# Kernel tuning notes

Hardware: AMD Instinct MI355X
Metric: run time of the kernel (lower is better)

Reference implementation:

```python
import jax, jax.numpy as jnp
import numpy as np
from jax import lax

TEMPERATURE = 0.0005


def conv1d(x, w, b, pad):
    # x: [B, Cin, T], w: [Cout, Cin, K], b: [Cout]
    y = lax.conv_general_dilated(x, w, window_strides=(1,), padding=[(pad, pad)],
                                 dimension_numbers=('NCH', 'OIH', 'NCH'))
    return y + b[None, :, None]


def setup_inputs() -> dict:
    key = jax.random.key(0)
    ks = jax.random.split(key, 16)
    B, Cq, Ck, Ca, Tde, Ten = 32, 80, 512, 80, 2000, 400

    def xavier(k, shape):
        fan_in = shape[1] * (shape[2] if len(shape) > 2 else 1)
        fan_out = shape[0] * (shape[2] if len(shape) > 2 else 1)
        lim = float(np.sqrt(6.0 / (fan_in + fan_out)))
        return jax.random.uniform(k, shape, jnp.float32, -lim, lim)

    inp = {
        'queries': jax.random.normal(ks[0], (B, Cq, Tde), jnp.float32),
        'keys': jax.random.normal(ks[1], (B, Ck, Ten), jnp.float32),
        'mask': jnp.ones((B, 1, Ten), jnp.int32),
        # key_layer: Conv(512->1024,k3,p1) -> ReLU -> Conv(1024->80,k1)
        'kw1': xavier(ks[2], (Ck * 2, Ck, 3)), 'kb1': jnp.zeros((Ck * 2,), jnp.float32),
        'kw2': xavier(ks[3], (Ca, Ck * 2, 1)), 'kb2': jnp.zeros((Ca,), jnp.float32),
        # query_layer: Conv(80->160,k3,p1)->ReLU->Conv(160->80,k1)->ReLU->Conv(80->80,k1)
        'qw1': xavier(ks[4], (Cq * 2, Cq, 3)), 'qb1': jnp.zeros((Cq * 2,), jnp.float32),
        'qw2': xavier(ks[5], (Cq, Cq * 2, 1)), 'qb2': jnp.zeros((Cq,), jnp.float32),
        'qw3': xavier(ks[6], (Ca, Cq, 1)), 'qb3': jnp.zeros((Ca,), jnp.float32),
    }
    return inp


def reference(queries, keys, mask, kw1, kb1, kw2, kb2, qw1, qb1, qw2, qb2, qw3, qb3):
    # key path: conv3 -> relu -> conv1
    k = conv1d(jax.nn.relu(conv1d(keys, kw1, kb1, 1)), kw2, kb2, 0)          # [B,Ca,Ten]
    # query path: conv3 -> relu -> conv1 -> relu -> conv1
    q = conv1d(queries, qw1, qb1, 1)
    q = jax.nn.relu(conv1d(jax.nn.relu(q), qw2, qb2, 0))
    q = conv1d(q, qw3, qb3, 0)                                               # [B,Ca,Tde]

    # sum_c (q - k)^2 = |q|^2 + |k|^2 - 2 q.k  (avoids [B,C,Tde,Ten] intermediate)
    q2 = jnp.sum(q * q, axis=1)                      # [B,Tde]
    k2 = jnp.sum(k * k, axis=1)                      # [B,Ten]
    qk = jnp.einsum('bcd,bce->bde', q, k)            # [B,Tde,Ten]
    dist = q2[:, :, None] + k2[:, None, :] - 2.0 * qk
    attn_logp = (-TEMPERATURE * dist)[:, None]       # [B,1,Tde,Ten]

    # masked fill over encoder positions (softmax dim)
    m = mask.astype(bool)[:, :, None, :]             # [B,1,1,Ten]
    attn_logp = jnp.where(m, attn_logp, -jnp.inf)
    attn = jax.nn.softmax(attn_logp, axis=3)
    return attn, attn_logp
```

## Files before the change

kernel.cpp:

```cpp
#include <hip/hip_runtime.h>
#include <hip/hip_bf16.h>
#include <math.h>

#define NB 32
#define CK 512
#define C1 1024
#define CA 80
#define CQ 80
#define CQ2 160
#define TEN 400
#define TDE 2000
#define KDIM 1536
#define TPAD 448
#define TQP 2048

static constexpr float TEMP = 0.0005f;

typedef __attribute__((ext_vector_type(8))) short short8;
typedef __attribute__((ext_vector_type(4))) float f32x4;

__device__ inline short f2bf(float v) {
  __hip_bfloat16 h = __float2bfloat16(v);
  return *(short*)&h;
}
__device__ inline float bf2f(short s) {
  __hip_bfloat16 h = *(__hip_bfloat16*)&s;
  return __bfloat162float(h);
}

__device__ inline void gload_lds16(const void* g, void* l) {
  __builtin_amdgcn_global_load_lds(
      (const __attribute__((address_space(1))) unsigned int*)g,
      (__attribute__((address_space(3))) unsigned int*)l, 16, 0, 0);
}


__device__ void cvt_weights_body(
    int i0, const float* __restrict__ kw1, const float* __restrict__ kw2,
    const float* __restrict__ qw1, const float* __restrict__ qw2,
    const float* __restrict__ qw3, short* __restrict__ w1bf,
    short* __restrict__ w2bf, short* __restrict__ w1q,
    short* __restrict__ w2q, short* __restrict__ w3q) {
  int i = i0 * 256 + threadIdx.x;
  if (i < 1572864) {
    w1bf[i] = f2bf(kw1[i]);
    return;
  }
  i -= 1572864;
  if (i < 131072) {
    int r = i >> 10, c = i & 1023;
    w2bf[i] = f2bf(r < CA ? kw2[r * 1024 + c] : 0.f);
    return;
  }
  i -= 131072;
  if (i < 49152) {
    int r = i >> 8, c = i & 255;
    w1q[i] = f2bf((r < CQ2 && c < 240) ? qw1[r * 240 + c] : 0.f);
    return;
  }
  i -= 49152;
  if (i < 20480) {
    int r = i / 160, c = i - r * 160;
    w2q[i] = f2bf(r < CA ? qw2[r * 160 + c] : 0.f);
    return;
  }
  i -= 20480;
  if (i < 12288) {
    int r = i / 96, c = i - r * 96;
    w3q[i] = f2bf((r < CA && c < CQ) ? qw3[r * 80 + c] : 0.f);
  }
}

__device__ void im2col_k_body(int idx, const float* __restrict__ keys,
                              short* __restrict__ BmatT, float* sq ) {
  const int t0 = (idx % 7) * 64;
  const int b = idx / 7;
  const int tid = threadIdx.x;
  for (int ci0 = 0; ci0 < CK; ci0 += 64) {
    for (int k = tid; k < 64 * 66; k += 256) {
      int c = k / 66, j = k % 66;
      int t = t0 - 1 + j;
      sq[c * 66 + j] =
          (t >= 0 && t < TEN) ? keys[((size_t)b * CK + ci0 + c) * TEN + t] : 0.f;
    }
    __syncthreads();
    for (int k = tid; k < 64 * 24; k += 256) {
      int j = k / 24, seg = k % 24;
      if (t0 + j < TEN) {
        short8 v;
        #pragma unroll
        for (int u = 0; u < 8; ++u) {
          int kk = seg * 8 + u;
          int ci = kk / 3, dk = kk - ci * 3;
          v[u] = f2bf(sq[ci * 66 + j + dk]);
        }
        *(short8*)(BmatT + ((size_t)b * TPAD + t0 + j) * KDIM + ci0 * 3 + seg * 8) = v;
      }
    }
    __syncthreads();
  }
}

__device__ void im2col_q_body(int idx, const float* __restrict__ queries,
                              short* __restrict__ Bq, float* sq ) {
  const int t0 = (idx & 31) * 64;
  const int b = idx >> 5;
  const int tid = threadIdx.x;
  for (int k = tid; k < 80 * 66; k += 256) {
    int c = k / 66, j = k % 66;
    int t = t0 - 1 + j;
    sq[c * 66 + j] =
        (t >= 0 && t < TDE) ? queries[((size_t)b * CQ + c) * TDE + t] : 0.f;
  }
  __syncthreads();
  for (int k = tid; k < 64 * 32; k += 256) {
    int j = k >> 5, seg = k & 31;
    const bool live = (t0 + j) < TDE;
    short8 v;
    #pragma unroll
    for (int u = 0; u < 8; ++u) {
      int kk = seg * 8 + u;
      float f = 0.f;
      if (live && kk < 240) {
        int ci = kk / 3, dk = kk - ci * 3;
        f = sq[ci * 66 + j + dk];
      }
      v[u] = f2bf(f);
    }
    *(short8*)(Bq + ((size_t)b * TQP + t0 + j) * 256 + seg * 8) = v;
  }
}

template <int MODE, bool RELU>
__device__ void qgemm_body(int bx, int by, int bz,
                           const short* __restrict__ A, const short* __restrict__ B,
                           const float* __restrict__ bias, void* __restrict__ outv,
                           int M, int Kpad, int kiters, int Nvalid, int outCols,
                           size_t bBatchStride, size_t outBatchStride, int outLD,
                           short* A_lds , short* B_lds ) {
  const int co0 = bx * 64;
  const int t0  = by * 64;
  const int b   = bz;
  const int tid = threadIdx.x;
  const int l = tid & 63, w = tid >> 6;
  const int srow = tid >> 2, sslot = tid & 3;

  const short* gA = A + (size_t)(co0 + srow) * Kpad + sslot * 8;
  const short* gB = B + (size_t)b * bBatchStride + (size_t)(t0 + srow) * Kpad + sslot * 8;
  const int wbyte = (srow * 64 + sslot * 16) ^ ((srow & 7) << 4);

  const int kslot = l >> 4;
  const int arow = w * 16 + (l & 15);
  const int abyte = (arow * 64 + kslot * 16) ^ ((arow & 7) << 4);
  int bbyte[4];
  #pragma unroll
  for (int g = 0; g < 4; ++g) {
    int brow = g * 16 + (l & 15);
    bbyte[g] = (brow * 64 + kslot * 16) ^ ((brow & 7) << 4);
  }

  f32x4 acc[4];
  #pragma unroll
  for (int g = 0; g < 4; ++g) acc[g] = (f32x4){0.f, 0.f, 0.f, 0.f};

  uint4 av = *(const uint4*)gA;
  uint4 bv = *(const uint4*)gB;
  for (int kt = 0; kt < kiters; ++kt) {
    __syncthreads();
    *(uint4*)((char*)A_lds + wbyte) = av;
    *(uint4*)((char*)B_lds + wbyte) = bv;
    __syncthreads();
    uint4 an = av, bn = bv;
    if (kt + 1 < kiters) {
      an = *(const uint4*)(gA + (kt + 1) * 32);
      bn = *(const uint4*)(gB + (kt + 1) * 32);
    }
    short8 a = *(const short8*)((const char*)A_lds + abyte);
    #pragma unroll
    for (int g = 0; g < 4; ++g) {
      short8 bb = *(const short8*)((const char*)B_lds + bbyte[g]);
      acc[g] = __builtin_amdgcn_mfma_f32_16x16x32_bf16(a, bb, acc[g], 0, 0, 0);
    }
    av = an; bv = bn;
  }

  #pragma unroll
  for (int g = 0; g < 4; ++g) {
    int t = t0 + g * 16 + (l & 15);
    if (t >= Nvalid) continue;
    #pragma unroll
    for (int r = 0; r < 4; ++r) {
      int co = co0 + w * 16 + kslot * 4 + r;
      if (MODE == 1) {
        if (co < outCols) {
          float v = 0.f;
          if (co < M) {
            v = acc[g][r] + bias[co];
            if (RELU) v = v > 0.f ? v : 0.f;
          }
          ((short*)outv)[(size_t)b * outBatchStride + (size_t)t * outLD + co] = f2bf(v);
        }
      } else {
        if (co < M) {
          float v = acc[g][r] + bias[co];
          if (RELU) v = v > 0.f ? v : 0.f;
          ((float*)outv)[(size_t)b * outBatchStride + (size_t)co * outLD + t] = v;
        }
      }
    }
  }
}


__global__ __launch_bounds__(256) void stageA_kernel(
    const float* __restrict__ kw1, const float* __restrict__ kw2,
    const float* __restrict__ qw1, const float* __restrict__ qw2,
    const float* __restrict__ qw3, short* __restrict__ w1bf,
    short* __restrict__ w2bf, short* __restrict__ w1q,
    short* __restrict__ w2q, short* __restrict__ w3q,
    const float* __restrict__ keys, short* __restrict__ BmatT) {
  __shared__ float sq[64 * 66];
  int flat = blockIdx.x;
  if (flat < 6976) {
    cvt_weights_body(flat, kw1, kw2, qw1, qw2, qw3, w1bf, w2bf, w1q, w2q, w3q);
  } else {
    im2col_k_body(flat - 6976, keys, BmatT, sq);
  }
}

__global__ __launch_bounds__(256) void kconv1_mfma_kernel(
    const short* __restrict__ w1bf, const short* __restrict__ BmatT,
    const float* __restrict__ b1, short* __restrict__ k1t) {
  __shared__ short A_lds[8192];
  __shared__ short B_lds[8192];
  const int flat = blockIdx.x;
  const int cox = flat >> 7;
  const int rem = flat & 127;
  const int b   = rem >> 2;
  const int ty  = rem & 3;
  const int co0 = cox * 128;
  const int t0  = ty * 128;
  const int tid = threadIdx.x;
  const int l = tid & 63, w = tid >> 6;

  const short* gsrc[8];
  short* ldst[8];
  #pragma unroll
  for (int j = 0; j < 8; ++j) {
    int c = w * 8 + j;
    int Y = (c & 15) * 1024 + l * 16;
    int X = Y ^ (((Y >> 7) & 7) << 4);
    int row = X >> 7, slot = (X >> 4) & 7;
    if (c < 16) {
      gsrc[j] = w1bf + (size_t)(co0 + row) * KDIM + slot * 8;
      ldst[j] = &A_lds[(c & 15) * 512];
    } else {
      int gr = t0 + row;
      if (gr > TPAD - 1) gr = TPAD - 1;
      gsrc[j] = BmatT + ((size_t)b * TPAD + gr) * KDIM + slot * 8;
      ldst[j] = &B_lds[(c & 15) * 512];
    }
  }

  const int kslot = l >> 4;
  const int li15 = l & 15;
  int abyte[2][2], bbyte[8][2];
  #pragma unroll
  for (int i = 0; i < 2; ++i) {
    int arow = w * 32 + i * 16 + li15;
    #pragma unroll
    for (int kk = 0; kk < 2; ++kk)
      abyte[i][kk] = (arow * 128 + kk * 64 + kslot * 16) ^ ((arow & 7) << 4);
  }
  #pragma unroll
  for (int g = 0; g < 8; ++g) {
    int brow = g * 16 + li15;
    #pragma unroll
    for (int kk = 0; kk < 2; ++kk)
      bbyte[g][kk] = (brow * 128 + kk * 64 + kslot * 16) ^ ((brow & 7) << 4);
  }

  f32x4 acc[2][8];
  #pragma unroll
  for (int i = 0; i < 2; ++i)
    #pragma unroll
    for (int g = 0; g < 8; ++g) acc[i][g] = (f32x4){0.f, 0.f, 0.f, 0.f};

  for (int kt = 0; kt < KDIM / 64; ++kt) {
    __syncthreads();
    #pragma unroll
    for (int j = 0; j < 8; ++j) gload_lds16(gsrc[j] + kt * 64, ldst[j]);
    __syncthreads();
    #pragma unroll
    for (int kk = 0; kk < 2; ++kk) {
      short8 a0 = *(const short8*)((const char*)A_lds + abyte[0][kk]);
      short8 a1 = *(const short8*)((const char*)A_lds + abyte[1][kk]);
      #pragma unroll
      for (int g = 0; g < 8; ++g) {
        short8 bb = *(const short8*)((const char*)B_lds + bbyte[g][kk]);
        acc[0][g] = __builtin_amdgcn_mfma_f32_16x16x32_bf16(a0, bb, acc[0][g], 0, 0, 0);
        acc[1][g] = __builtin_amdgcn_mfma_f32_16x16x32_bf16(a1, bb, acc[1][g], 0, 0, 0);
      }
    }
  }

  #pragma unroll
  for (int g = 0; g < 8; ++g) {
    int t = t0 + g * 16 + li15;
    if (t < TEN) {
      #pragma unroll
      for (int i = 0; i < 2; ++i) {
        #pragma unroll
        for (int r = 0; r < 4; ++r) {
          int co = co0 + w * 32 + i * 16 + kslot * 4 + r;
          float v = acc[i][g][r] + b1[co];
          k1t[((size_t)b * TPAD + t) * C1 + co] = f2bf(v > 0.f ? v : 0.f);
        }
      }
    }
  }
}

__global__ __launch_bounds__(256) void stageC_kernel(
    const float* __restrict__ queries, short* __restrict__ Bq,
    const short* __restrict__ w2bf, const short* __restrict__ k1t,
    const float* __restrict__ kb2, short* __restrict__ kB) {
  __shared__ __align__(16) char pool[21120];
  int flat = blockIdx.x;
  if (flat < 1024) {
    im2col_q_body(flat, queries, Bq, (float*)pool);
  } else {
    int j = flat - 1024;
    int bx = j & 1, rest = j >> 1;
    int by = rest % 7, bz = rest / 7;
    qgemm_body<1, false>(bx, by, bz, w2bf, k1t, kb2, kB, CA, C1, 32, TEN, 96,
                         (size_t)TPAD * C1, (size_t)TPAD * 96, 96,
                         (short*)pool, (short*)(pool + 4096));
  }
}

template <int MODE, bool RELU>
__global__ __launch_bounds__(256) void qgemm_kernel(
    const short* __restrict__ A, const short* __restrict__ B,
    const float* __restrict__ bias, void* __restrict__ outv,
    int M, int Kpad, int kiters, int Nvalid, int outCols,
    size_t bBatchStride, size_t outBatchStride, int outLD) {
  __shared__ short A_lds[2048];
  __shared__ short B_lds[2048];
  qgemm_body<MODE, RELU>(blockIdx.x, blockIdx.y, blockIdx.z, A, B, bias, outv,
                         M, Kpad, kiters, Nvalid, outCols, bBatchStride,
                         outBatchStride, outLD, A_lds, B_lds);
}

__global__ __launch_bounds__(256) void attn_fused_kernel(
    const short* __restrict__ qA, const short* __restrict__ kB,
    const int* __restrict__ mask, float* __restrict__ out_attn,
    float* __restrict__ out_logp) {
  __shared__ short A_lds[3][2048];
  __shared__ short B_lds[3][2560];
  __shared__ float k2LDS[400];
  __shared__ float q2row[64];
  __shared__ int mLDS[400];
  const int t0 = blockIdx.x * 64;
  const int b  = blockIdx.y;
  const int tid = threadIdx.x;
  const int l = tid & 63, w = tid >> 6;

  {
    const int arow_s = tid >> 2, aslot = tid & 3;
    const short* gA = qA + ((size_t)b * TQP + t0 + arow_s) * 96 + aslot * 8;
    #pragma unroll
    for (int p = 0; p < 3; ++p) {
      uint4 v = *(const uint4*)(gA + p * 32);
      *(uint4*)((char*)&A_lds[p][0] +
                ((arow_s * 64 + aslot * 16) ^ ((arow_s & 7) << 4))) = v;
    }
  }
  for (int idx = tid; idx < 400; idx += 256) {
    mLDS[idx] = mask[(size_t)b * TEN + idx];
  }

  const int kslot = l >> 4;
  const int arow = w * 16 + (l & 15);
  const int abyte = (arow * 64 + kslot * 16) ^ ((arow & 7) << 4);

  f32x4 acc[25];
  #pragma unroll
  for (int i = 0; i < 25; ++i) acc[i] = (f32x4){0.f, 0.f, 0.f, 0.f};

  __syncthreads();

  {
    int row = tid >> 2, g = tid & 3;
    float s = 0.f;
    #pragma unroll
    for (int q3i = 0; q3i < 3; ++q3i) {
      int q = 3 * g + q3i;
      int p = q >> 2, slot = q & 3;
      int byteo = (row * 64 + slot * 16) ^ ((row & 7) << 4);
      short8 v = *(const short8*)((const char*)&A_lds[p][0] + byteo);
      #pragma unroll
      for (int u = 0; u < 8; ++u) { float f = bf2f(v[u]); s += f * f; }
    }
    s += __shfl_xor(s, 1, 64);
    s += __shfl_xor(s, 2, 64);
    if (g == 0) q2row[row] = s;
  }

  #pragma unroll
  for (int st = 0; st < 5; ++st) {
    for (int idx = tid; idx < 960; idx += 256) {
      int row = idx / 12, c = idx - row * 12;
      int panel = c >> 2, ps = c & 3;
      uint4 v = *(const uint4*)(kB + ((size_t)b * TPAD + st * 80 + row) * 96 + c * 8);
      *(uint4*)((char*)&B_lds[panel][0] +
                ((row * 64 + ps * 16) ^ ((row & 7) << 4))) = v;
    }
    __syncthreads();
    if (tid < 160) {
      int row = tid >> 1, h = tid & 1;
      float s = 0.f;
      #pragma unroll
      for (int qi = 0; qi < 6; ++qi) {
        int q = 6 * h + qi;
        int p = q >> 2, slot = q & 3;
        int byteo = (row * 64 + slot * 16) ^ ((row & 7) << 4);
        short8 v = *(const short8*)((const char*)&B_lds[p][0] + byteo);
        #pragma unroll
        for (int u = 0; u < 8; ++u) { float f = bf2f(v[u]); s += f * f; }
      }
      s += __shfl_xor(s, 1, 64);
      if (h == 0) k2LDS[st * 80 + row] = s;
    }
    #pragma unroll
    for (int kt = 0; kt < 3; ++kt) {
      short8 a = *(const short8*)((const char*)&A_lds[kt][0] + abyte);
      #pragma unroll
      for (int f = 0; f < 5; ++f) {
        int brow = f * 16 + (l & 15);
        short8 bb = *(const short8*)((const char*)&B_lds[kt][0] +
                                     ((brow * 64 + kslot * 16) ^ ((brow & 7) << 4)));
        acc[st * 5 + f] =
            __builtin_amdgcn_mfma_f32_16x16x32_bf16(a, bb, acc[st * 5 + f], 0, 0, 0);
      }
    }
    __syncthreads();
  }

  int trow[4]; float q2v[4];
  #pragma unroll
  for (int r = 0; r < 4; ++r) {
    trow[r] = t0 + w * 16 + kslot * 4 + r;
    q2v[r] = q2row[w * 16 + kslot * 4 + r];
  }
  #pragma unroll
  for (int sf = 0; sf < 25; ++sf) {
    int s = sf * 16 + (l & 15);
    float k2v = k2LDS[s];
    bool mk = mLDS[s] != 0;
    #pragma unroll
    for (int r = 0; r < 4; ++r) {
      float lp = mk ? (-TEMP) * (q2v[r] + k2v - 2.f * acc[sf][r]) : -INFINITY;
      acc[sf][r] = lp;
    }
  }
  #pragma unroll
  for (int r = 0; r < 4; ++r) {
    if (trow[r] < TDE) {
      float* dst = out_logp + ((size_t)(b * TDE + trow[r])) * TEN + (l & 15);
      #pragma unroll
      for (int sf = 0; sf < 25; ++sf) dst[sf * 16] = acc[sf][r];
    }
  }
  float m[4];
  #pragma unroll
  for (int r = 0; r < 4; ++r) m[r] = -INFINITY;
  #pragma unroll
  for (int sf = 0; sf < 25; ++sf)
    #pragma unroll
    for (int r = 0; r < 4; ++r) m[r] = fmaxf(m[r], acc[sf][r]);
  #pragma unroll
  for (int o = 1; o < 16; o <<= 1)
    #pragma unroll
    for (int r = 0; r < 4; ++r) m[r] = fmaxf(m[r], __shfl_xor(m[r], o, 64));
  float sum[4] = {0.f, 0.f, 0.f, 0.f};
  #pragma unroll
  for (int sf = 0; sf < 25; ++sf)
    #pragma unroll
    for (int r = 0; r < 4; ++r) {
      float v = acc[sf][r];
      float e = (v != -INFINITY) ? __expf(v - m[r]) : 0.f;
      acc[sf][r] = e;
      sum[r] += e;
    }
  #pragma unroll
  for (int o = 1; o < 16; o <<= 1)
    #pragma unroll
    for (int r = 0; r < 4; ++r) sum[r] += __shfl_xor(sum[r], o, 64);
  float inv[4];
  #pragma unroll
  for (int r = 0; r < 4; ++r) inv[r] = 1.0f / sum[r];
  #pragma unroll
  for (int r = 0; r < 4; ++r) {
    if (trow[r] < TDE) {
      float* dst = out_attn + ((size_t)(b * TDE + trow[r])) * TEN + (l & 15);
      #pragma unroll
      for (int sf = 0; sf < 25; ++sf) dst[sf * 16] = acc[sf][r] * inv[r];
    }
  }
}

extern "C" void kernel_launch(void* const* d_in, const int* in_sizes, int n_in,
                              void* d_out, int out_size, void* d_ws, size_t ws_size,
                              hipStream_t stream) {
  const float* queries = (const float*)d_in[0];
  const float* keys    = (const float*)d_in[1];
  const int*   mask    = (const int*)d_in[2];
  const float* kw1 = (const float*)d_in[3];
  const float* kb1 = (const float*)d_in[4];
  const float* kw2 = (const float*)d_in[5];
  const float* kb2 = (const float*)d_in[6];
  const float* qw1 = (const float*)d_in[7];
  const float* qb1 = (const float*)d_in[8];
  const float* qw2 = (const float*)d_in[9];
  const float* qb2 = (const float*)d_in[10];
  const float* qw3 = (const float*)d_in[11];
  const float* qb3 = (const float*)d_in[12];
  float* out = (float*)d_out;

  char* ws = (char*)d_ws;
  short* BmatT = (short*)ws;
  short* w1bf  = (short*)(ws + 44040192);
  short* k1t   = (short*)(ws + 47185920);
  short* w2bf  = (short*)(ws + 76546048);
  short* w1q   = (short*)(ws + 76808192);
  short* w2q   = (short*)(ws + 76906496);
  short* w3q   = (short*)(ws + 76947456);
  short* Bq    = (short*)ws;
  short* q1bf  = (short*)(ws + 33554432);
  short* q2bf  = (short*)(ws + 54525952);
  short* qA    = (short*)(ws + 20480000);
  short* kB    = (short*)(ws + 81920000);

  const long long HALF = 25600000LL;
  float* out_attn = out;
  float* out_logp = out + HALF;

  stageA_kernel<<<dim3(7200), dim3(256), 0, stream>>>(
      kw1, kw2, qw1, qw2, qw3, w1bf, w2bf, w1q, w2q, w3q, keys, BmatT);

  kconv1_mfma_kernel<<<dim3(1024), dim3(256), 0, stream>>>(w1bf, BmatT, kb1, k1t);

  stageC_kernel<<<dim3(1472), dim3(256), 0, stream>>>(
      queries, Bq, w2bf, k1t, kb2, kB);

  qgemm_kernel<1, true><<<dim3(3, TQP / 64, NB), dim3(256), 0, stream>>>(
      w1q, Bq, qb1, q1bf, CQ2, 256, 8, TQP, 160,
      (size_t)TQP * 256, (size_t)TQP * 160, 160);
  qgemm_kernel<1, true><<<dim3(2, TQP / 64, NB), dim3(256), 0, stream>>>(
      w2q, q1bf, qb2, q2bf, CA, 160, 5, TQP, 96,
      (size_t)TQP * 160, (size_t)TQP * 96, 96);
  qgemm_kernel<1, false><<<dim3(2, TQP / 64, NB), dim3(256), 0, stream>>>(
      w3q, q2bf, qb3, qA, CA, 96, 3, TQP, 96,
      (size_t)TQP * 96, (size_t)TQP * 96, 96);

  attn_fused_kernel<<<dim3(TQP / 64, NB), dim3(256), 0, stream>>>(
      qA, kB, mask, out_attn, out_logp);
}
```

Measured before the change: 329.6 us.

## Double-buffer LDS tiles in key conv1 GEMM with halved K step

The key-path conv1 MFMA kernel now keeps two LDS buffers for the A and B tiles. Global-to-LDS loads for the next K slice are issued while MFMAs run on the current one, so each iteration needs one barrier instead of two. The K step drops from 64 to 32 to keep LDS use the same. The XOR swizzle and its inverse are rewritten for the narrower 64-byte rows. In exchange there are twice as many loop iterations, each with less work to hide the barrier and load latency behind.

```diff
diff --git a/kernel.cpp b/kernel.cpp
--- a/kernel.cpp
+++ b/kernel.cpp
@@ -231,8 +231,8 @@
 __global__ __launch_bounds__(256) void kconv1_mfma_kernel(
     const short* __restrict__ w1bf, const short* __restrict__ BmatT,
     const float* __restrict__ b1, short* __restrict__ k1t) {
-  __shared__ short A_lds[8192];
-  __shared__ short B_lds[8192];
+  __shared__ short A_lds[2][4096];
+  __shared__ short B_lds[2][4096];
   const int flat = blockIdx.x;
   const int cox = flat >> 7;
   const int rem = flat & 127;
@@ -243,41 +243,47 @@
   const int tid = threadIdx.x;
   const int l = tid & 63, w = tid >> 6;
 
-  const short* gsrc[8];
-  short* ldst[8];
-  #pragma unroll
-  for (int j = 0; j < 8; ++j) {
-    int c = w * 8 + j;
-    int Y = (c & 15) * 1024 + l * 16;
-    int X = Y ^ (((Y >> 7) & 7) << 4);
-    int row = X >> 7, slot = (X >> 4) & 7;
-    if (c < 16) {
+  auto invswz = [](int Y) {
+    int X = Y;
+    X ^= ((Y >> 8) & 1) << 6;
+    X ^= ((Y >> 7) & 1) << 5;
+    X ^= (((Y >> 6) ^ (Y >> 8)) & 1) << 4;
+    return X;
+  };
+
+  const short* gsrc[4];
+  int ldoff[4];
+  bool isA[4];
+  #pragma unroll
+  for (int j = 0; j < 4; ++j) {
+    int c = w * 4 + j;
+    int Y = (c & 7) * 1024 + l * 16;
+    int X = invswz(Y);
+    int row = X >> 6, slot = (X >> 4) & 3;
+    isA[j] = (c < 8);
+    ldoff[j] = (c & 7) * 512;
+    if (c < 8) {
       gsrc[j] = w1bf + (size_t)(co0 + row) * KDIM + slot * 8;
-      ldst[j] = &A_lds[(c & 15) * 512];
     } else {
       int gr = t0 + row;
       if (gr > TPAD - 1) gr = TPAD - 1;
       gsrc[j] = BmatT + ((size_t)b * TPAD + gr) * KDIM + slot * 8;
-      ldst[j] = &B_lds[(c & 15) * 512];
     }
   }
 
   const int kslot = l >> 4;
   const int li15 = l & 15;
-  int abyte[2][2], bbyte[8][2];
+  int abyte[2];
   #pragma unroll
   for (int i = 0; i < 2; ++i) {
     int arow = w * 32 + i * 16 + li15;
-    #pragma unroll
-    for (int kk = 0; kk < 2; ++kk)
-      abyte[i][kk] = (arow * 128 + kk * 64 + kslot * 16) ^ ((arow & 7) << 4);
-  }
+    abyte[i] = (arow * 64 + kslot * 16) ^ ((arow & 7) << 4);
+  }
+  int bbyte[8];
   #pragma unroll
   for (int g = 0; g < 8; ++g) {
     int brow = g * 16 + li15;
-    #pragma unroll
-    for (int kk = 0; kk < 2; ++kk)
-      bbyte[g][kk] = (brow * 128 + kk * 64 + kslot * 16) ^ ((brow & 7) << 4);
+    bbyte[g] = (brow * 64 + kslot * 16) ^ ((brow & 7) << 4);
   }
 
   f32x4 acc[2][8];
@@ -286,22 +292,32 @@
     #pragma unroll
     for (int g = 0; g < 8; ++g) acc[i][g] = (f32x4){0.f, 0.f, 0.f, 0.f};
 
-  for (int kt = 0; kt < KDIM / 64; ++kt) {
-    __syncthreads();
-    #pragma unroll
-    for (int j = 0; j < 8; ++j) gload_lds16(gsrc[j] + kt * 64, ldst[j]);
-    __syncthreads();
-    #pragma unroll
-    for (int kk = 0; kk < 2; ++kk) {
-      short8 a0 = *(const short8*)((const char*)A_lds + abyte[0][kk]);
-      short8 a1 = *(const short8*)((const char*)A_lds + abyte[1][kk]);
-      #pragma unroll
-      for (int g = 0; g < 8; ++g) {
-        short8 bb = *(const short8*)((const char*)B_lds + bbyte[g][kk]);
-        acc[0][g] = __builtin_amdgcn_mfma_f32_16x16x32_bf16(a0, bb, acc[0][g], 0, 0, 0);
-        acc[1][g] = __builtin_amdgcn_mfma_f32_16x16x32_bf16(a1, bb, acc[1][g], 0, 0, 0);
-      }
-    }
+  #pragma unroll
+  for (int j = 0; j < 4; ++j)
+    gload_lds16(gsrc[j], (isA[j] ? &A_lds[0][0] : &B_lds[0][0]) + ldoff[j]);
+  __syncthreads();
+
+  int cur = 0;
+  for (int kt = 0; kt < KDIM / 32; ++kt) {
+    if (kt + 1 < KDIM / 32) {
+      int nxt = cur ^ 1;
+      #pragma unroll
+      for (int j = 0; j < 4; ++j)
+        gload_lds16(gsrc[j] + (kt + 1) * 32,
+                    (isA[j] ? &A_lds[nxt][0] : &B_lds[nxt][0]) + ldoff[j]);
+    }
+    const char* Abase = (const char*)&A_lds[cur][0];
+    const char* Bbase = (const char*)&B_lds[cur][0];
+    short8 a0 = *(const short8*)(Abase + abyte[0]);
+    short8 a1 = *(const short8*)(Abase + abyte[1]);
+    #pragma unroll
+    for (int g = 0; g < 8; ++g) {
+      short8 bb = *(const short8*)(Bbase + bbyte[g]);
+      acc[0][g] = __builtin_amdgcn_mfma_f32_16x16x32_bf16(a0, bb, acc[0][g], 0, 0, 0);
+      acc[1][g] = __builtin_amdgcn_mfma_f32_16x16x32_bf16(a1, bb, acc[1][g], 0, 0, 0);
+    }
+    __syncthreads();
+    cur ^= 1;
   }
 
   #pragma unroll
```

New measurement: 343.4 us. +4.2%, slower.
